# Kernel optimization log

Hardware: AMD Instinct MI355X
Metric: run time of the kernel (lower is better)

The kernel has to match this reference:

```python
import jax, jax.numpy as jnp
import numpy as np

DMODEL, DK, HEADS, FF = 512, 64, 8, 2048
HD = HEADS * DK  # 512; heads are NOT split in this module
EPS = 1e-5


def layernorm(x, g, b):
    mu = jnp.mean(x, axis=-1, keepdims=True)
    var = jnp.mean(jnp.square(x - mu), axis=-1, keepdims=True)
    return (x - mu) * jax.lax.rsqrt(var + EPS) * g + b


def setup_inputs() -> dict:
    key = jax.random.key(0)
    ks = jax.random.split(key, 20)
    s = 1.0 / np.sqrt(DMODEL)
    u = lambda k, shape, fan: jax.random.uniform(k, shape, jnp.float32, -1.0 / np.sqrt(fan), 1.0 / np.sqrt(fan))
    return {
        "x": jax.random.normal(ks[0], (4, 4096, DMODEL), jnp.float32),
        "Wq_w": u(ks[1], (DMODEL, HD), DMODEL), "Wq_b": u(ks[2], (HD,), DMODEL),
        "Wk_w": u(ks[3], (DMODEL, HD), DMODEL), "Wk_b": u(ks[4], (HD,), DMODEL),
        "Wv_w": u(ks[5], (DMODEL, HD), DMODEL), "Wv_b": u(ks[6], (HD,), DMODEL),
        "Wu_w": u(ks[7], (HD, DMODEL), HD), "Wu_b": u(ks[8], (DMODEL,), HD),
        "ln1_g": jnp.ones((DMODEL,), jnp.float32), "ln1_b": jnp.zeros((DMODEL,), jnp.float32),
        "ff1_w": u(ks[9], (DMODEL, FF), DMODEL), "ff1_b": u(ks[10], (FF,), DMODEL),
        "ff2_w": u(ks[11], (FF, DMODEL), FF), "ff2_b": u(ks[12], (DMODEL,), FF),
        "ln2_g": jnp.ones((DMODEL,), jnp.float32), "ln2_b": jnp.zeros((DMODEL,), jnp.float32),
    }


def reference(x, Wq_w, Wq_b, Wk_w, Wk_b, Wv_w, Wv_b, Wu_w, Wu_b,
              ln1_g, ln1_b, ff1_w, ff1_b, ff2_w, ff2_b, ln2_g, ln2_b):
    # x: (b, n, dmodel). Single encoder layer, faithful to num_encoders=1.
    q = x @ Wq_w + Wq_b            # (b, n, HD)
    k = x @ Wk_w + Wk_b
    v = x @ Wv_w + Wv_b
    # NOTE: original does bmm over full HD dim (no head split), scaled by sqrt(dk)
    scores = jnp.einsum('bnd,bmd->bnm', q, k) / np.sqrt(DK)
    probs = jax.nn.softmax(scores, axis=-1)   # (b, n, n) — O(n^2) materialized as in source
    attn = jnp.einsum('bnm,bmd->bnd', probs, v)
    unified = attn @ Wu_w + Wu_b
    h = layernorm(x + unified, ln1_g, ln1_b)
    ffwd = jax.nn.relu(h @ ff1_w + ff1_b) @ ff2_w + ff2_b
    return layernorm(h + ffwd, ln2_g, ln2_b)
```

## Files before the change

kernel.cpp:

```cpp
#include <hip/hip_runtime.h>

#define AS1 __attribute__((address_space(1)))
#define AS3 __attribute__((address_space(3)))

typedef __attribute__((ext_vector_type(8))) short short8;
typedef __attribute__((ext_vector_type(4))) float floatx4;

__device__ __forceinline__ float b2f(ushort u) {
  union { unsigned int i; float f; } x; x.i = ((unsigned int)u) << 16; return x.f;
}
__device__ __forceinline__ ushort f2b(float f) {
  union { float f; unsigned int i; } x; x.f = f;
  unsigned int r = (x.i + 0x7fffu + ((x.i >> 16) & 1u)) >> 16;
  return (ushort)r;
}

#define GF_RELU 1


__global__ __launch_bounds__(256) void gemm_vw(
    const ushort* __restrict__ qkv, const ushort* __restrict__ wut,
    ushort* __restrict__ vwt)
{
  __shared__ __align__(16) ushort As[128 * 32];
  __shared__ __align__(16) ushort Bs[128 * 32];

  const int id = blockIdx.x;
  const int b  = id >> 7;
  const int t  = id & 127;
  const int bx = t & 31;
  const int by = t >> 5;

  const ushort* A  = wut;
  const ushort* Bt = qkv + (size_t)b * 4096 * 1536 + 1024;
  ushort* C = vwt + (size_t)b * 512 * 4096;

  const int tid  = threadIdx.x;
  const int w    = tid >> 6;
  const int lane = tid & 63;
  const int lo   = lane & 15;
  const int quad = lane >> 4;
  const int m0   = by * 128;
  const int n0   = bx * 128;
  const int wm   = (w & 1) * 64;
  const int wn   = (w >> 1) * 64;

  const int i0 = tid, i1 = tid + 256;
  const ushort* ga0 = A  + (size_t)(m0 + (i0 >> 2)) * 512 + ((i0 & 3) << 3);
  const ushort* ga1 = A  + (size_t)(m0 + (i1 >> 2)) * 512 + ((i1 & 3) << 3);
  const ushort* gb0 = Bt + (size_t)(n0 + (i0 >> 2)) * 1536 + ((i0 & 3) << 3);
  const ushort* gb1 = Bt + (size_t)(n0 + (i1 >> 2)) * 1536 + ((i1 & 3) << 3);

  floatx4 acc[4][4] = {};

  for (int k0 = 0; k0 < 512; k0 += 32) {
    __syncthreads();
    __builtin_amdgcn_global_load_lds((const AS1 void*)(ga0 + k0), (AS3 void*)(As + i0 * 8), 16, 0, 0);
    __builtin_amdgcn_global_load_lds((const AS1 void*)(ga1 + k0), (AS3 void*)(As + i1 * 8), 16, 0, 0);
    __builtin_amdgcn_global_load_lds((const AS1 void*)(gb0 + k0), (AS3 void*)(Bs + i0 * 8), 16, 0, 0);
    __builtin_amdgcn_global_load_lds((const AS1 void*)(gb1 + k0), (AS3 void*)(Bs + i1 * 8), 16, 0, 0);
    __syncthreads();

    short8 af[4], bf[4];
#pragma unroll
    for (int tt = 0; tt < 4; ++tt) {
      af[tt] = *(const short8*)(As + (wm + tt * 16 + lo) * 32 + quad * 8);
      bf[tt] = *(const short8*)(Bs + (wn + tt * 16 + lo) * 32 + quad * 8);
    }
#pragma unroll
    for (int mt = 0; mt < 4; ++mt)
#pragma unroll
      for (int nt = 0; nt < 4; ++nt)
        acc[mt][nt] = __builtin_amdgcn_mfma_f32_16x16x32_bf16(af[mt], bf[nt], acc[mt][nt], 0, 0, 0);
  }

#pragma unroll
  for (int mt = 0; mt < 4; ++mt)
#pragma unroll
    for (int nt = 0; nt < 4; ++nt)
#pragma unroll
      for (int r = 0; r < 4; ++r) {
        const int row = m0 + wm + mt * 16 + quad * 4 + r;
        const int col = n0 + wn + nt * 16 + lo;
        C[(size_t)row * 4096 + col] = f2b(acc[mt][nt][r]);
      }
}

__global__ __launch_bounds__(256) void gemm_qk_exp(
    const ushort* __restrict__ qkv, ushort* __restrict__ P)
{
  __shared__ __align__(16) ushort smem[128 * 128];
  ushort* As = smem;
  ushort* Bs = smem + 128 * 64;

  const int id  = blockIdx.x;
  const int xcd = id & 7;
  const int s   = id >> 3;
  const int b   = xcd >> 1;
  const int by  = (xcd & 1) * 16 + (s & 15);
  const int bx  = s >> 4;

  const ushort* A  = qkv + (size_t)b * 4096 * 1536;
  const ushort* Bt = qkv + (size_t)b * 4096 * 1536 + 512;
  ushort* C = P + (size_t)b * 4096 * 4096;

  const int tid  = threadIdx.x;
  const int w    = tid >> 6;
  const int lane = tid & 63;
  const int lo   = lane & 15;
  const int quad = lane >> 4;
  const int m0   = by * 128;
  const int n0   = bx * 128;
  const int wm   = (w & 1) * 64;
  const int wn   = (w >> 1) * 64;

  const ushort* gaP[4]; const ushort* gbP[4];
#pragma unroll
  for (int k = 0; k < 4; ++k) {
    const int s_ = tid + k * 256;
    const int row = s_ >> 3, sl = s_ & 7;
    gaP[k] = A  + (size_t)(m0 + row) * 1536 + ((sl ^ (row & 7)) << 3);
    gbP[k] = Bt + (size_t)(n0 + row) * 1536 + ((sl ^ (row & 7)) << 3);
  }

  floatx4 acc[4][4] = {};

  for (int k0 = 0; k0 < 512; k0 += 64) {
    __syncthreads();
#pragma unroll
    for (int k = 0; k < 4; ++k) {
      const int s_ = tid + k * 256;
      __builtin_amdgcn_global_load_lds((const AS1 void*)(gaP[k] + k0), (AS3 void*)(As + s_ * 8), 16, 0, 0);
      __builtin_amdgcn_global_load_lds((const AS1 void*)(gbP[k] + k0), (AS3 void*)(Bs + s_ * 8), 16, 0, 0);
    }
    __syncthreads();

#pragma unroll
    for (int kk = 0; kk < 2; ++kk) {
      short8 af[4], bf[4];
#pragma unroll
      for (int tt = 0; tt < 4; ++tt) {
        const int ra = wm + tt * 16 + lo;
        const int rb = wn + tt * 16 + lo;
        af[tt] = *(const short8*)(As + (size_t)ra * 64 + (((kk * 4 + quad) ^ (ra & 7)) << 3));
        bf[tt] = *(const short8*)(Bs + (size_t)rb * 64 + (((kk * 4 + quad) ^ (rb & 7)) << 3));
      }
#pragma unroll
      for (int mt = 0; mt < 4; ++mt)
#pragma unroll
        for (int nt = 0; nt < 4; ++nt)
          acc[mt][nt] = __builtin_amdgcn_mfma_f32_16x16x32_bf16(af[mt], bf[nt], acc[mt][nt], 0, 0, 0);
    }
  }

  __syncthreads();
#pragma unroll
  for (int mt = 0; mt < 4; ++mt)
#pragma unroll
    for (int r = 0; r < 4; ++r) {
      const int row = wm + mt * 16 + quad * 4 + r;
#pragma unroll
      for (int nt = 0; nt < 4; ++nt) {
        const int col = wn + nt * 16 + lo;
        smem[row * 128 + ((((col >> 3) ^ (row & 7)) << 3) | (col & 7))] =
            f2b(__expf(acc[mt][nt][r] * 0.125f));
      }
    }
  __syncthreads();
#pragma unroll
  for (int k = 0; k < 8; ++k) {
    const int c = tid + k * 256;
    const int row = c >> 4, c16 = c & 15;
    const short8 v = *(const short8*)(smem + row * 128 + ((c16 ^ (row & 7)) << 3));
    *(short8*)(C + (size_t)(m0 + row) * 4096 + n0 + c16 * 8) = v;
  }
}

__global__ __launch_bounds__(256) void gemm_pv_wu(
    const ushort* __restrict__ P, const ushort* __restrict__ vwt,
    const float* __restrict__ bias, ushort* __restrict__ uni)
{
  __shared__ __align__(16) ushort As[128 * 64];
  __shared__ __align__(16) ushort Bs[128 * 64];
  __shared__ float rsm[128];

  const int id  = blockIdx.x;
  const int xcd = id & 7;
  const int s   = id >> 3;
  const int bx  = s & 3;
  const int panel = xcd * 16 + (s >> 2);
  const int b  = panel >> 5;
  const int by = panel & 31;

  const ushort* A  = P   + (size_t)b * 4096 * 4096;
  const ushort* Bt = vwt + (size_t)b * 512 * 4096;

  const int tid  = threadIdx.x;
  const int w    = tid >> 6;
  const int lane = tid & 63;
  const int lo   = lane & 15;
  const int quad = lane >> 4;
  const int m0   = by * 128;
  const int n0   = bx * 128;
  const int wm   = (w & 1) * 64;
  const int wn   = (w >> 1) * 64;

  const ushort* gaP[4]; const ushort* gbP[4];
#pragma unroll
  for (int k = 0; k < 4; ++k) {
    const int s_ = tid + k * 256;
    const int row = s_ >> 3, sl = s_ & 7;
    gaP[k] = A  + (size_t)(m0 + row) * 4096 + ((sl ^ (row & 7)) << 3);
    gbP[k] = Bt + (size_t)(n0 + row) * 4096 + ((sl ^ (row & 7)) << 3);
  }

  short8 ones;
#pragma unroll
  for (int j = 0; j < 8; ++j) ones[j] = (short)0x3F80;

  floatx4 acc[4][4] = {};
  floatx4 rsacc[4] = {};

  for (int k0 = 0; k0 < 4096; k0 += 64) {
    __syncthreads();
#pragma unroll
    for (int k = 0; k < 4; ++k) {
      const int s_ = tid + k * 256;
      __builtin_amdgcn_global_load_lds((const AS1 void*)(gaP[k] + k0), (AS3 void*)(As + s_ * 8), 16, 0, 0);
      __builtin_amdgcn_global_load_lds((const AS1 void*)(gbP[k] + k0), (AS3 void*)(Bs + s_ * 8), 16, 0, 0);
    }
    __syncthreads();

#pragma unroll
    for (int kk = 0; kk < 2; ++kk) {
      short8 af[4], bf[4];
#pragma unroll
      for (int tt = 0; tt < 4; ++tt) {
        const int ra = wm + tt * 16 + lo;
        const int rb = wn + tt * 16 + lo;
        af[tt] = *(const short8*)(As + (size_t)ra * 64 + (((kk * 4 + quad) ^ (ra & 7)) << 3));
        bf[tt] = *(const short8*)(Bs + (size_t)rb * 64 + (((kk * 4 + quad) ^ (rb & 7)) << 3));
      }
#pragma unroll
      for (int tt = 0; tt < 4; ++tt)
        rsacc[tt] = __builtin_amdgcn_mfma_f32_16x16x32_bf16(af[tt], ones, rsacc[tt], 0, 0, 0);
#pragma unroll
      for (int mt = 0; mt < 4; ++mt)
#pragma unroll
        for (int nt = 0; nt < 4; ++nt)
          acc[mt][nt] = __builtin_amdgcn_mfma_f32_16x16x32_bf16(af[mt], bf[nt], acc[mt][nt], 0, 0, 0);
    }
  }

  if (wn == 0 && lo == 0) {
#pragma unroll
    for (int tt = 0; tt < 4; ++tt)
#pragma unroll
      for (int r = 0; r < 4; ++r)
        rsm[wm + tt * 16 + quad * 4 + r] = rsacc[tt][r];
  }
  __syncthreads();

#pragma unroll
  for (int mt = 0; mt < 4; ++mt)
#pragma unroll
    for (int r = 0; r < 4; ++r) {
      const int lrow = wm + mt * 16 + quad * 4 + r;
      const size_t grow = (size_t)b * 4096 + m0 + lrow;
      const float inv = 1.f / rsm[lrow];
#pragma unroll
      for (int nt = 0; nt < 4; ++nt) {
        const int col = n0 + wn + nt * 16 + lo;
        uni[grow * 512 + col] = f2b(acc[mt][nt][r] * inv + bias[col]);
      }
    }
}

__global__ __launch_bounds__(256) void gemm_async64(
    const ushort* __restrict__ A, const ushort* __restrict__ Bt,
    const float* __restrict__ bias, ushort* __restrict__ C,
    int N, int K, int lda, int ldb,
    int lg_gx, int lg_gy, float scale, int flags)
{
  __shared__ __align__(16) ushort smem[128 * 128];
  ushort* As = smem;
  ushort* Bs = smem + 128 * 64;

  const int id = blockIdx.x;
  const int r8 = id & 7;
  const int s  = id >> 3;
  const int bx = s & ((1 << lg_gx) - 1);
  const int j  = r8 + ((s >> lg_gx) << 3);
  const int by = j & ((1 << lg_gy) - 1);

  const int tid  = threadIdx.x;
  const int w    = tid >> 6;
  const int lane = tid & 63;
  const int lo   = lane & 15;
  const int quad = lane >> 4;
  const int m0   = by * 128;
  const int n0   = bx * 128;
  const int wm   = (w & 1) * 64;
  const int wn   = (w >> 1) * 64;

  const ushort* gaP[4]; const ushort* gbP[4];
#pragma unroll
  for (int k = 0; k < 4; ++k) {
    const int s_ = tid + k * 256;
    const int row = s_ >> 3, sl = s_ & 7;
    gaP[k] = A  + (size_t)(m0 + row) * lda + ((sl ^ (row & 7)) << 3);
    gbP[k] = Bt + (size_t)(n0 + row) * ldb + ((sl ^ (row & 7)) << 3);
  }

  floatx4 acc[4][4] = {};

  for (int k0 = 0; k0 < K; k0 += 64) {
    __syncthreads();
#pragma unroll
    for (int k = 0; k < 4; ++k) {
      const int s_ = tid + k * 256;
      __builtin_amdgcn_global_load_lds((const AS1 void*)(gaP[k] + k0), (AS3 void*)(As + s_ * 8), 16, 0, 0);
      __builtin_amdgcn_global_load_lds((const AS1 void*)(gbP[k] + k0), (AS3 void*)(Bs + s_ * 8), 16, 0, 0);
    }
    __syncthreads();

#pragma unroll
    for (int kk = 0; kk < 2; ++kk) {
      short8 af[4], bf[4];
#pragma unroll
      for (int tt = 0; tt < 4; ++tt) {
        const int ra = wm + tt * 16 + lo;
        const int rb = wn + tt * 16 + lo;
        af[tt] = *(const short8*)(As + (size_t)ra * 64 + (((kk * 4 + quad) ^ (ra & 7)) << 3));
        bf[tt] = *(const short8*)(Bs + (size_t)rb * 64 + (((kk * 4 + quad) ^ (rb & 7)) << 3));
      }
#pragma unroll
      for (int mt = 0; mt < 4; ++mt)
#pragma unroll
        for (int nt = 0; nt < 4; ++nt)
          acc[mt][nt] = __builtin_amdgcn_mfma_f32_16x16x32_bf16(af[mt], bf[nt], acc[mt][nt], 0, 0, 0);
    }
  }

  __syncthreads();
#pragma unroll
  for (int mt = 0; mt < 4; ++mt)
#pragma unroll
    for (int r = 0; r < 4; ++r) {
      const int row = wm + mt * 16 + quad * 4 + r;
#pragma unroll
      for (int nt = 0; nt < 4; ++nt) {
        const int col = wn + nt * 16 + lo;
        float v = acc[mt][nt][r] * scale;
        if (bias) v += bias[n0 + col];
        if (flags & GF_RELU) v = fmaxf(v, 0.f);
        smem[row * 128 + ((((col >> 3) ^ (row & 7)) << 3) | (col & 7))] = f2b(v);
      }
    }
  __syncthreads();
#pragma unroll
  for (int k = 0; k < 8; ++k) {
    const int c = tid + k * 256;
    const int row = c >> 4, c16 = c & 15;
    const short8 v = *(const short8*)(smem + row * 128 + ((c16 ^ (row & 7)) << 3));
    *(short8*)(C + (size_t)(m0 + row) * N + n0 + c16 * 8) = v;
  }
}

__global__ __launch_bounds__(256) void gemm_qkv(
    const ushort* __restrict__ A, const ushort* __restrict__ Bt,
    const float* __restrict__ bias, ushort* __restrict__ C)
{
  __shared__ __align__(16) ushort smem[128 * 128];
  ushort* As = smem;
  ushort* Bs = smem + 128 * 64;

  const int bx = blockIdx.x;
  const int by = blockIdx.y;

  const int tid  = threadIdx.x;
  const int w    = tid >> 6;
  const int lane = tid & 63;
  const int lo   = lane & 15;
  const int quad = lane >> 4;
  const int m0   = by * 128;
  const int n0   = bx * 128;
  const int wm   = (w & 1) * 64;
  const int wn   = (w >> 1) * 64;

  const ushort* gaP[4]; const ushort* gbP[4];
#pragma unroll
  for (int k = 0; k < 4; ++k) {
    const int s_ = tid + k * 256;
    const int row = s_ >> 3, sl = s_ & 7;
    gaP[k] = A  + (size_t)(m0 + row) * 512 + ((sl ^ (row & 7)) << 3);
    gbP[k] = Bt + (size_t)(n0 + row) * 512 + ((sl ^ (row & 7)) << 3);
  }

  floatx4 acc[4][4] = {};

  for (int k0 = 0; k0 < 512; k0 += 64) {
    __syncthreads();
#pragma unroll
    for (int k = 0; k < 4; ++k) {
      const int s_ = tid + k * 256;
      __builtin_amdgcn_global_load_lds((const AS1 void*)(gaP[k] + k0), (AS3 void*)(As + s_ * 8), 16, 0, 0);
      __builtin_amdgcn_global_load_lds((const AS1 void*)(gbP[k] + k0), (AS3 void*)(Bs + s_ * 8), 16, 0, 0);
    }
    __syncthreads();

#pragma unroll
    for (int kk = 0; kk < 2; ++kk) {
      short8 af[4], bf[4];
#pragma unroll
      for (int tt = 0; tt < 4; ++tt) {
        const int ra = wm + tt * 16 + lo;
        const int rb = wn + tt * 16 + lo;
        af[tt] = *(const short8*)(As + (size_t)ra * 64 + (((kk * 4 + quad) ^ (ra & 7)) << 3));
        bf[tt] = *(const short8*)(Bs + (size_t)rb * 64 + (((kk * 4 + quad) ^ (rb & 7)) << 3));
      }
#pragma unroll
      for (int mt = 0; mt < 4; ++mt)
#pragma unroll
        for (int nt = 0; nt < 4; ++nt)
          acc[mt][nt] = __builtin_amdgcn_mfma_f32_16x16x32_bf16(af[mt], bf[nt], acc[mt][nt], 0, 0, 0);
    }
  }

  __syncthreads();
#pragma unroll
  for (int mt = 0; mt < 4; ++mt)
#pragma unroll
    for (int r = 0; r < 4; ++r) {
      const int row = wm + mt * 16 + quad * 4 + r;
#pragma unroll
      for (int nt = 0; nt < 4; ++nt) {
        const int col = wn + nt * 16 + lo;
        smem[row * 128 + ((((col >> 3) ^ (row & 7)) << 3) | (col & 7))] =
            f2b(acc[mt][nt][r] + bias[n0 + col]);
      }
    }
  __syncthreads();
#pragma unroll
  for (int k = 0; k < 8; ++k) {
    const int c = tid + k * 256;
    const int row = c >> 4, c16 = c & 15;
    const short8 v = *(const short8*)(smem + row * 128 + ((c16 ^ (row & 7)) << 3));
    *(short8*)(C + (size_t)(m0 + row) * 1536 + n0 + c16 * 8) = v;
  }
}

__global__ __launch_bounds__(256) void cast_f32_bf16(
    const float* __restrict__ in, ushort* __restrict__ out)
{
  const size_t i = ((size_t)blockIdx.x * 256 + threadIdx.x) * 8;
  const float4 a = *(const float4*)(in + i);
  const float4 b = *(const float4*)(in + i + 4);
  short8 v;
  v[0] = (short)f2b(a.x); v[1] = (short)f2b(a.y);
  v[2] = (short)f2b(a.z); v[3] = (short)f2b(a.w);
  v[4] = (short)f2b(b.x); v[5] = (short)f2b(b.y);
  v[6] = (short)f2b(b.z); v[7] = (short)f2b(b.w);
  *(short8*)(out + i) = v;
}

__global__ void transpose_cast(const float* __restrict__ in, ushort* __restrict__ out,
                               int R, int C)
{
  __shared__ ushort t[64][65];
  const int r0 = blockIdx.y * 64, c0 = blockIdx.x * 64;
  const int tx = threadIdx.x, ty = threadIdx.y;
  for (int i = ty; i < 64; i += 4)
    t[i][tx] = f2b(in[(size_t)(r0 + i) * C + c0 + tx]);
  __syncthreads();
  for (int i = ty; i < 64; i += 4)
    out[(size_t)(c0 + i) * R + r0 + tx] = t[tx][i];
}

__global__ void concat_bias(const float* __restrict__ a, const float* __restrict__ b,
                            const float* __restrict__ c, float* __restrict__ o)
{
  const int i = blockIdx.x * 256 + threadIdx.x;
  o[i] = (i < 512) ? a[i] : ((i < 1024) ? b[i - 512] : c[i - 1024]);
}

__global__ __launch_bounds__(256) void ln_res(
    const void* __restrict__ Xv, int x_f32, const ushort* __restrict__ Y,
    const float* __restrict__ g, const float* __restrict__ b,
    void* __restrict__ outv, int o_f32)
{
  const int w = threadIdx.x >> 6, lane = threadIdx.x & 63;
  const size_t row = (size_t)blockIdx.x * 4 + w;
  const size_t base = row * 512 + lane * 8;

  float v[8];
  if (x_f32) {
    const float* X = (const float*)Xv + base;
    const float4 x0 = *(const float4*)(X), x1 = *(const float4*)(X + 4);
    v[0] = x0.x; v[1] = x0.y; v[2] = x0.z; v[3] = x0.w;
    v[4] = x1.x; v[5] = x1.y; v[6] = x1.z; v[7] = x1.w;
  } else {
    const short8 xv = *(const short8*)((const ushort*)Xv + base);
#pragma unroll
    for (int j = 0; j < 8; ++j) v[j] = b2f((ushort)xv[j]);
  }
  const short8 yv = *(const short8*)(Y + base);
  float s = 0.f, sq = 0.f;
#pragma unroll
  for (int j = 0; j < 8; ++j) {
    v[j] += b2f((ushort)yv[j]);
    s += v[j]; sq += v[j] * v[j];
  }
  for (int m = 1; m < 64; m <<= 1) {
    s  += __shfl_xor(s,  m, 64);
    sq += __shfl_xor(sq, m, 64);
  }
  const float mean = s * (1.f / 512.f);
  const float var  = sq * (1.f / 512.f) - mean * mean;
  const float rstd = rsqrtf(fmaxf(var, 0.f) + 1e-5f);

  const float4 g0 = *(const float4*)(g + lane * 8);
  const float4 g1 = *(const float4*)(g + lane * 8 + 4);
  const float4 b0 = *(const float4*)(b + lane * 8);
  const float4 b1 = *(const float4*)(b + lane * 8 + 4);
  const float gg[8] = {g0.x, g0.y, g0.z, g0.w, g1.x, g1.y, g1.z, g1.w};
  const float bb[8] = {b0.x, b0.y, b0.z, b0.w, b1.x, b1.y, b1.z, b1.w};

  if (o_f32) {
    float* o = (float*)outv + base;
#pragma unroll
    for (int j = 0; j < 8; ++j) o[j] = (v[j] - mean) * rstd * gg[j] + bb[j];
  } else {
    ushort* o = (ushort*)outv + base;
    short8 ov;
#pragma unroll
    for (int j = 0; j < 8; ++j) ov[j] = (short)f2b((v[j] - mean) * rstd * gg[j] + bb[j]);
    *(short8*)o = ov;
  }
}

extern "C" void kernel_launch(void* const* d_in, const int* in_sizes, int n_in,
                              void* d_out, int out_size, void* d_ws, size_t ws_size,
                              hipStream_t stream)
{
  const float* x    = (const float*)d_in[0];
  const float* Wq_w = (const float*)d_in[1];
  const float* Wq_b = (const float*)d_in[2];
  const float* Wk_w = (const float*)d_in[3];
  const float* Wk_b = (const float*)d_in[4];
  const float* Wv_w = (const float*)d_in[5];
  const float* Wv_b = (const float*)d_in[6];
  const float* Wu_w = (const float*)d_in[7];
  const float* Wu_b = (const float*)d_in[8];
  const float* g1   = (const float*)d_in[9];
  const float* b1   = (const float*)d_in[10];
  const float* f1w  = (const float*)d_in[11];
  const float* f1b  = (const float*)d_in[12];
  const float* f2w  = (const float*)d_in[13];
  const float* f2bv = (const float*)d_in[14];
  const float* g2   = (const float*)d_in[15];
  const float* b2   = (const float*)d_in[16];

  char* wsb = (char*)d_ws;
  ushort* wqkvt = (ushort*)(wsb + 0);
  ushort* wut   = (ushort*)(wsb + 1572864);
  ushort* f1t   = (ushort*)(wsb + 2097152);
  ushort* f2t   = (ushort*)(wsb + 4194304);
  float*  bqkv  = (float*) (wsb + 6291456);
  ushort* qkv   = (ushort*)(wsb + 6297600);
  ushort* vwt   = (ushort*)(wsb + 56629248);
  ushort* uni   = (ushort*)(wsb + 73406464);
  ushort* h     = (ushort*)(wsb + 106960896);
  ushort* mid   = (ushort*)(wsb + 123738112);
  ushort* ffo   = (ushort*)(wsb + 190846976);
  ushort* Pbuf  = (ushort*)(wsb + 90183680);
  ushort* xb    = (ushort*)(wsb + 90183680);

  const dim3 tb(64, 4);
  transpose_cast<<<dim3(8, 8),  tb, 0, stream>>>(Wq_w, wqkvt,              512, 512);
  transpose_cast<<<dim3(8, 8),  tb, 0, stream>>>(Wk_w, wqkvt + 512 * 512,  512, 512);
  transpose_cast<<<dim3(8, 8),  tb, 0, stream>>>(Wv_w, wqkvt + 1024 * 512, 512, 512);
  transpose_cast<<<dim3(8, 8),  tb, 0, stream>>>(Wu_w, wut, 512, 512);
  transpose_cast<<<dim3(32, 8), tb, 0, stream>>>(f1w, f1t, 512, 2048);
  transpose_cast<<<dim3(8, 32), tb, 0, stream>>>(f2w, f2t, 2048, 512);
  concat_bias<<<6, 256, 0, stream>>>(Wq_b, Wk_b, Wv_b, bqkv);

  cast_f32_bf16<<<4096, 256, 0, stream>>>(x, xb);
  gemm_qkv<<<dim3(12, 128), 256, 0, stream>>>(xb, wqkvt, bqkv, qkv);

  gemm_vw<<<512, 256, 0, stream>>>(qkv, wut, vwt);
  gemm_qk_exp<<<4096, 256, 0, stream>>>(qkv, Pbuf);
  gemm_pv_wu<<<512, 256, 0, stream>>>(Pbuf, vwt, Wu_b, uni);

  ln_res<<<4096, 256, 0, stream>>>(x, 1, uni, g1, b1, h, 0);

  gemm_async64<<<2048, 256, 0, stream>>>(h, f1t, f1b, mid,
      2048, 512, 512, 512, 4, 7, 1.f, GF_RELU);
  gemm_async64<<<512, 256, 0, stream>>>(mid, f2t, f2bv, ffo,
      512, 2048, 2048, 2048, 2, 7, 1.f, 0);
  ln_res<<<4096, 256, 0, stream>>>(h, 0, ffo, g2, b2, d_out, 1);
}
```

Before: 512.0 us.

## Double-buffer LDS tiles in GEMM kernels to overlap loads with MFMA

Four GEMM kernels (QK-exp, PV-Wu, the generic async GEMM, and QKV) now use two LDS buffers for the A/B tiles. The next K-tile is issued with global_load_lds while MFMAs run on the current buffer, and the two barriers per iteration drop to one. The goal is to hide global-load latency behind compute. LDS per block doubles to 64 KB, which may lower occupancy, and correctness depends on the single barrier ordering the async LDS writes.

```diff
diff --git a/kernel.cpp b/kernel.cpp
--- a/kernel.cpp
+++ b/kernel.cpp
@@ -89,9 +89,7 @@
 __global__ __launch_bounds__(256) void gemm_qk_exp(
     const ushort* __restrict__ qkv, ushort* __restrict__ P)
 {
-  __shared__ __align__(16) ushort smem[128 * 128];
-  ushort* As = smem;
-  ushort* Bs = smem + 128 * 64;
+  __shared__ __align__(16) ushort smem[4 * 128 * 64];
 
   const int id  = blockIdx.x;
   const int xcd = id & 7;
@@ -125,15 +123,30 @@
 
   floatx4 acc[4][4] = {};
 
-  for (int k0 = 0; k0 < 512; k0 += 64) {
-    __syncthreads();
-#pragma unroll
-    for (int k = 0; k < 4; ++k) {
-      const int s_ = tid + k * 256;
-      __builtin_amdgcn_global_load_lds((const AS1 void*)(gaP[k] + k0), (AS3 void*)(As + s_ * 8), 16, 0, 0);
-      __builtin_amdgcn_global_load_lds((const AS1 void*)(gbP[k] + k0), (AS3 void*)(Bs + s_ * 8), 16, 0, 0);
-    }
-    __syncthreads();
+#pragma unroll
+  for (int k = 0; k < 4; ++k) {
+    const int s_ = tid + k * 256;
+    __builtin_amdgcn_global_load_lds((const AS1 void*)(gaP[k]), (AS3 void*)(smem + s_ * 8), 16, 0, 0);
+    __builtin_amdgcn_global_load_lds((const AS1 void*)(gbP[k]), (AS3 void*)(smem + 8192 + s_ * 8), 16, 0, 0);
+  }
+  __syncthreads();
+
+  for (int it = 0; it < 8; ++it) {
+    const int bo = (it & 1) << 14;
+    const ushort* Ac = smem + bo;
+    const ushort* Bc = smem + bo + 8192;
+    if (it < 7) {
+      const int bn = ((it & 1) ^ 1) << 14;
+      ushort* An = smem + bn;
+      ushort* Bn = smem + bn + 8192;
+      const int k0n = (it + 1) * 64;
+#pragma unroll
+      for (int k = 0; k < 4; ++k) {
+        const int s_ = tid + k * 256;
+        __builtin_amdgcn_global_load_lds((const AS1 void*)(gaP[k] + k0n), (AS3 void*)(An + s_ * 8), 16, 0, 0);
+        __builtin_amdgcn_global_load_lds((const AS1 void*)(gbP[k] + k0n), (AS3 void*)(Bn + s_ * 8), 16, 0, 0);
+      }
+    }
 
 #pragma unroll
     for (int kk = 0; kk < 2; ++kk) {
@@ -142,8 +155,8 @@
       for (int tt = 0; tt < 4; ++tt) {
         const int ra = wm + tt * 16 + lo;
         const int rb = wn + tt * 16 + lo;
-        af[tt] = *(const short8*)(As + (size_t)ra * 64 + (((kk * 4 + quad) ^ (ra & 7)) << 3));
-        bf[tt] = *(const short8*)(Bs + (size_t)rb * 64 + (((kk * 4 + quad) ^ (rb & 7)) << 3));
+        af[tt] = *(const short8*)(Ac + (size_t)ra * 64 + (((kk * 4 + quad) ^ (ra & 7)) << 3));
+        bf[tt] = *(const short8*)(Bc + (size_t)rb * 64 + (((kk * 4 + quad) ^ (rb & 7)) << 3));
       }
 #pragma unroll
       for (int mt = 0; mt < 4; ++mt)
@@ -151,9 +164,9 @@
         for (int nt = 0; nt < 4; ++nt)
           acc[mt][nt] = __builtin_amdgcn_mfma_f32_16x16x32_bf16(af[mt], bf[nt], acc[mt][nt], 0, 0, 0);
     }
-  }
-
-  __syncthreads();
+    __syncthreads();
+  }
+
 #pragma unroll
   for (int mt = 0; mt < 4; ++mt)
 #pragma unroll
@@ -180,8 +193,7 @@
     const ushort* __restrict__ P, const ushort* __restrict__ vwt,
     const float* __restrict__ bias, ushort* __restrict__ uni)
 {
-  __shared__ __align__(16) ushort As[128 * 64];
-  __shared__ __align__(16) ushort Bs[128 * 64];
+  __shared__ __align__(16) ushort smem[4 * 128 * 64];
   __shared__ float rsm[128];
 
   const int id  = blockIdx.x;
@@ -221,15 +233,30 @@
   floatx4 acc[4][4] = {};
   floatx4 rsacc[4] = {};
 
-  for (int k0 = 0; k0 < 4096; k0 += 64) {
-    __syncthreads();
-#pragma unroll
-    for (int k = 0; k < 4; ++k) {
-      const int s_ = tid + k * 256;
-      __builtin_amdgcn_global_load_lds((const AS1 void*)(gaP[k] + k0), (AS3 void*)(As + s_ * 8), 16, 0, 0);
-      __builtin_amdgcn_global_load_lds((const AS1 void*)(gbP[k] + k0), (AS3 void*)(Bs + s_ * 8), 16, 0, 0);
-    }
-    __syncthreads();
+#pragma unroll
+  for (int k = 0; k < 4; ++k) {
+    const int s_ = tid + k * 256;
+    __builtin_amdgcn_global_load_lds((const AS1 void*)(gaP[k]), (AS3 void*)(smem + s_ * 8), 16, 0, 0);
+    __builtin_amdgcn_global_load_lds((const AS1 void*)(gbP[k]), (AS3 void*)(smem + 8192 + s_ * 8), 16, 0, 0);
+  }
+  __syncthreads();
+
+  for (int it = 0; it < 64; ++it) {
+    const int bo = (it & 1) << 14;
+    const ushort* Ac = smem + bo;
+    const ushort* Bc = smem + bo + 8192;
+    if (it < 63) {
+      const int bn = ((it & 1) ^ 1) << 14;
+      ushort* An = smem + bn;
+      ushort* Bn = smem + bn + 8192;
+      const int k0n = (it + 1) * 64;
+#pragma unroll
+      for (int k = 0; k < 4; ++k) {
+        const int s_ = tid + k * 256;
+        __builtin_amdgcn_global_load_lds((const AS1 void*)(gaP[k] + k0n), (AS3 void*)(An + s_ * 8), 16, 0, 0);
+        __builtin_amdgcn_global_load_lds((const AS1 void*)(gbP[k] + k0n), (AS3 void*)(Bn + s_ * 8), 16, 0, 0);
+      }
+    }
 
 #pragma unroll
     for (int kk = 0; kk < 2; ++kk) {
@@ -238,8 +265,8 @@
       for (int tt = 0; tt < 4; ++tt) {
         const int ra = wm + tt * 16 + lo;
         const int rb = wn + tt * 16 + lo;
-        af[tt] = *(const short8*)(As + (size_t)ra * 64 + (((kk * 4 + quad) ^ (ra & 7)) << 3));
-        bf[tt] = *(const short8*)(Bs + (size_t)rb * 64 + (((kk * 4 + quad) ^ (rb & 7)) << 3));
+        af[tt] = *(const short8*)(Ac + (size_t)ra * 64 + (((kk * 4 + quad) ^ (ra & 7)) << 3));
+        bf[tt] = *(const short8*)(Bc + (size_t)rb * 64 + (((kk * 4 + quad) ^ (rb & 7)) << 3));
       }
 #pragma unroll
       for (int tt = 0; tt < 4; ++tt)
@@ -250,6 +277,7 @@
         for (int nt = 0; nt < 4; ++nt)
           acc[mt][nt] = __builtin_amdgcn_mfma_f32_16x16x32_bf16(af[mt], bf[nt], acc[mt][nt], 0, 0, 0);
     }
+    __syncthreads();
   }
 
   if (wn == 0 && lo == 0) {
@@ -282,9 +310,7 @@
     int N, int K, int lda, int ldb,
     int lg_gx, int lg_gy, float scale, int flags)
 {
-  __shared__ __align__(16) ushort smem[128 * 128];
-  ushort* As = smem;
-  ushort* Bs = smem + 128 * 64;
+  __shared__ __align__(16) ushort smem[4 * 128 * 64];
 
   const int id = blockIdx.x;
   const int r8 = id & 7;
@@ -313,16 +339,32 @@
   }
 
   floatx4 acc[4][4] = {};
-
-  for (int k0 = 0; k0 < K; k0 += 64) {
-    __syncthreads();
-#pragma unroll
-    for (int k = 0; k < 4; ++k) {
-      const int s_ = tid + k * 256;
-      __builtin_amdgcn_global_load_lds((const AS1 void*)(gaP[k] + k0), (AS3 void*)(As + s_ * 8), 16, 0, 0);
-      __builtin_amdgcn_global_load_lds((const AS1 void*)(gbP[k] + k0), (AS3 void*)(Bs + s_ * 8), 16, 0, 0);
-    }
-    __syncthreads();
+  const int nt_ = K >> 6;
+
+#pragma unroll
+  for (int k = 0; k < 4; ++k) {
+    const int s_ = tid + k * 256;
+    __builtin_amdgcn_global_load_lds((const AS1 void*)(gaP[k]), (AS3 void*)(smem + s_ * 8), 16, 0, 0);
+    __builtin_amdgcn_global_load_lds((const AS1 void*)(gbP[k]), (AS3 void*)(smem + 8192 + s_ * 8), 16, 0, 0);
+  }
+  __syncthreads();
+
+  for (int it = 0; it < nt_; ++it) {
+    const int bo = (it & 1) << 14;
+    const ushort* Ac = smem + bo;
+    const ushort* Bc = smem + bo + 8192;
+    if (it + 1 < nt_) {
+      const int bn = ((it & 1) ^ 1) << 14;
+      ushort* An = smem + bn;
+      ushort* Bn = smem + bn + 8192;
+      const int k0n = (it + 1) * 64;
+#pragma unroll
+      for (int k = 0; k < 4; ++k) {
+        const int s_ = tid + k * 256;
+        __builtin_amdgcn_global_load_lds((const AS1 void*)(gaP[k] + k0n), (AS3 void*)(An + s_ * 8), 16, 0, 0);
+        __builtin_amdgcn_global_load_lds((const AS1 void*)(gbP[k] + k0n), (AS3 void*)(Bn + s_ * 8), 16, 0, 0);
+      }
+    }
 
 #pragma unroll
     for (int kk = 0; kk < 2; ++kk) {
@@ -331,8 +373,8 @@
       for (int tt = 0; tt < 4; ++tt) {
         const int ra = wm + tt * 16 + lo;
         const int rb = wn + tt * 16 + lo;
-        af[tt] = *(const short8*)(As + (size_t)ra * 64 + (((kk * 4 + quad) ^ (ra & 7)) << 3));
-        bf[tt] = *(const short8*)(Bs + (size_t)rb * 64 + (((kk * 4 + quad) ^ (rb & 7)) << 3));
+        af[tt] = *(const short8*)(Ac + (size_t)ra * 64 + (((kk * 4 + quad) ^ (ra & 7)) << 3));
+        bf[tt] = *(const short8*)(Bc + (size_t)rb * 64 + (((kk * 4 + quad) ^ (rb & 7)) << 3));
       }
 #pragma unroll
       for (int mt = 0; mt < 4; ++mt)
@@ -340,9 +382,9 @@
         for (int nt = 0; nt < 4; ++nt)
           acc[mt][nt] = __builtin_amdgcn_mfma_f32_16x16x32_bf16(af[mt], bf[nt], acc[mt][nt], 0, 0, 0);
     }
-  }
-
-  __syncthreads();
+    __syncthreads();
+  }
+
 #pragma unroll
   for (int mt = 0; mt < 4; ++mt)
 #pragma unroll
@@ -371,9 +413,7 @@
     const ushort* __restrict__ A, const ushort* __restrict__ Bt,
     const float* __restrict__ bias, ushort* __restrict__ C)
 {
-  __shared__ __align__(16) ushort smem[128 * 128];
-  ushort* As = smem;
-  ushort* Bs = smem + 128 * 64;
+  __shared__ __align__(16) ushort smem[4 * 128 * 64];
 
   const int bx = blockIdx.x;
   const int by = blockIdx.y;
@@ -399,15 +439,30 @@
 
   floatx4 acc[4][4] = {};
 
-  for (int k0 = 0; k0 < 512; k0 += 64) {
-    __syncthreads();
-#pragma unroll
-    for (int k = 0; k < 4; ++k) {
-      const int s_ = tid + k * 256;
-      __builtin_amdgcn_global_load_lds((const AS1 void*)(gaP[k] + k0), (AS3 void*)(As + s_ * 8), 16, 0, 0);
-      __builtin_amdgcn_global_load_lds((const AS1 void*)(gbP[k] + k0), (AS3 void*)(Bs + s_ * 8), 16, 0, 0);
-    }
-    __syncthreads();
+#pragma unroll
+  for (int k = 0; k < 4; ++k) {
+    const int s_ = tid + k * 256;
+    __builtin_amdgcn_global_load_lds((const AS1 void*)(gaP[k]), (AS3 void*)(smem + s_ * 8), 16, 0, 0);
+    __builtin_amdgcn_global_load_lds((const AS1 void*)(gbP[k]), (AS3 void*)(smem + 8192 + s_ * 8), 16, 0, 0);
+  }
+  __syncthreads();
+
+  for (int it = 0; it < 8; ++it) {
+    const int bo = (it & 1) << 14;
+    const ushort* Ac = smem + bo;
+    const ushort* Bc = smem + bo + 8192;
+    if (it < 7) {
+      const int bn = ((it & 1) ^ 1) << 14;
+      ushort* An = smem + bn;
+      ushort* Bn = smem + bn + 8192;
+      const int k0n = (it + 1) * 64;
+#pragma unroll
+      for (int k = 0; k < 4; ++k) {
+        const int s_ = tid + k * 256;
+        __builtin_amdgcn_global_load_lds((const AS1 void*)(gaP[k] + k0n), (AS3 void*)(An + s_ * 8), 16, 0, 0);
+        __builtin_amdgcn_global_load_lds((const AS1 void*)(gbP[k] + k0n), (AS3 void*)(Bn + s_ * 8), 16, 0, 0);
+      }
+    }
 
 #pragma unroll
     for (int kk = 0; kk < 2; ++kk) {
@@ -416,8 +471,8 @@
       for (int tt = 0; tt < 4; ++tt) {
         const int ra = wm + tt * 16 + lo;
         const int rb = wn + tt * 16 + lo;
-        af[tt] = *(const short8*)(As + (size_t)ra * 64 + (((kk * 4 + quad) ^ (ra & 7)) << 3));
-        bf[tt] = *(const short8*)(Bs + (size_t)rb * 64 + (((kk * 4 + quad) ^ (rb & 7)) << 3));
+        af[tt] = *(const short8*)(Ac + (size_t)ra * 64 + (((kk * 4 + quad) ^ (ra & 7)) << 3));
+        bf[tt] = *(const short8*)(Bc + (size_t)rb * 64 + (((kk * 4 + quad) ^ (rb & 7)) << 3));
       }
 #pragma unroll
       for (int mt = 0; mt < 4; ++mt)
@@ -425,9 +480,9 @@
         for (int nt = 0; nt < 4; ++nt)
           acc[mt][nt] = __builtin_amdgcn_mfma_f32_16x16x32_bf16(af[mt], bf[nt], acc[mt][nt], 0, 0, 0);
     }
-  }
-
-  __syncthreads();
+    __syncthreads();
+  }
+
 #pragma unroll
   for (int mt = 0; mt < 4; ++mt)
 #pragma unroll
```

New measurement: 540.7 us. 5.6% more time.

## Double-buffer LDS tiles in QK^T exp GEMM to overlap loads with MFMA

Applied to the files above, without the earlier changes.

The QK^T-plus-exp kernel now uses two LDS stage buffers. It prefetches the next K-slice of the A and B tiles with global_load_lds while MFMAs run on the current slice, and drops to one barrier per iteration. The aim is to hide global-memory latency behind compute. In exchange, LDS use per block doubles to 64KB, which can lower how many blocks fit on a CU.

```diff
diff --git a/kernel.cpp b/kernel.cpp
--- a/kernel.cpp
+++ b/kernel.cpp
@@ -89,9 +89,7 @@
 __global__ __launch_bounds__(256) void gemm_qk_exp(
     const ushort* __restrict__ qkv, ushort* __restrict__ P)
 {
-  __shared__ __align__(16) ushort smem[128 * 128];
-  ushort* As = smem;
-  ushort* Bs = smem + 128 * 64;
+  __shared__ __align__(16) ushort smem[4 * 128 * 64];
 
   const int id  = blockIdx.x;
   const int xcd = id & 7;
@@ -125,15 +123,30 @@
 
   floatx4 acc[4][4] = {};
 
-  for (int k0 = 0; k0 < 512; k0 += 64) {
-    __syncthreads();
-#pragma unroll
-    for (int k = 0; k < 4; ++k) {
-      const int s_ = tid + k * 256;
-      __builtin_amdgcn_global_load_lds((const AS1 void*)(gaP[k] + k0), (AS3 void*)(As + s_ * 8), 16, 0, 0);
-      __builtin_amdgcn_global_load_lds((const AS1 void*)(gbP[k] + k0), (AS3 void*)(Bs + s_ * 8), 16, 0, 0);
-    }
-    __syncthreads();
+#pragma unroll
+  for (int k = 0; k < 4; ++k) {
+    const int s_ = tid + k * 256;
+    __builtin_amdgcn_global_load_lds((const AS1 void*)(gaP[k]), (AS3 void*)(smem + s_ * 8), 16, 0, 0);
+    __builtin_amdgcn_global_load_lds((const AS1 void*)(gbP[k]), (AS3 void*)(smem + 8192 + s_ * 8), 16, 0, 0);
+  }
+  __syncthreads();
+
+  for (int it = 0; it < 8; ++it) {
+    const int bo = (it & 1) << 14;
+    const ushort* Ac = smem + bo;
+    const ushort* Bc = smem + bo + 8192;
+    if (it < 7) {
+      const int bn = ((it & 1) ^ 1) << 14;
+      ushort* An = smem + bn;
+      ushort* Bn = smem + bn + 8192;
+      const int k0n = (it + 1) * 64;
+#pragma unroll
+      for (int k = 0; k < 4; ++k) {
+        const int s_ = tid + k * 256;
+        __builtin_amdgcn_global_load_lds((const AS1 void*)(gaP[k] + k0n), (AS3 void*)(An + s_ * 8), 16, 0, 0);
+        __builtin_amdgcn_global_load_lds((const AS1 void*)(gbP[k] + k0n), (AS3 void*)(Bn + s_ * 8), 16, 0, 0);
+      }
+    }
 
 #pragma unroll
     for (int kk = 0; kk < 2; ++kk) {
@@ -142,8 +155,8 @@
       for (int tt = 0; tt < 4; ++tt) {
         const int ra = wm + tt * 16 + lo;
         const int rb = wn + tt * 16 + lo;
-        af[tt] = *(const short8*)(As + (size_t)ra * 64 + (((kk * 4 + quad) ^ (ra & 7)) << 3));
-        bf[tt] = *(const short8*)(Bs + (size_t)rb * 64 + (((kk * 4 + quad) ^ (rb & 7)) << 3));
+        af[tt] = *(const short8*)(Ac + (size_t)ra * 64 + (((kk * 4 + quad) ^ (ra & 7)) << 3));
+        bf[tt] = *(const short8*)(Bc + (size_t)rb * 64 + (((kk * 4 + quad) ^ (rb & 7)) << 3));
       }
 #pragma unroll
       for (int mt = 0; mt < 4; ++mt)
@@ -151,9 +164,9 @@
         for (int nt = 0; nt < 4; ++nt)
           acc[mt][nt] = __builtin_amdgcn_mfma_f32_16x16x32_bf16(af[mt], bf[nt], acc[mt][nt], 0, 0, 0);
     }
-  }
-
-  __syncthreads();
+    __syncthreads();
+  }
+
 #pragma unroll
   for (int mt = 0; mt < 4; ++mt)
 #pragma unroll
```

New measurement: 500.5 us. 2.2% less time.
